# Optimization experiments

Measured on AMD Instinct MI355X. Metric: run time of the kernel, lower is better.

The kernel has to match this reference:

```python
import jax, jax.numpy as jnp
import numpy as np

EPS = 1e-8

def rms_norm(x, g):
    xf = x.astype(jnp.float32)
    ms = jnp.mean(xf * xf, axis=-1, keepdims=True)
    return (g * (xf * jax.lax.rsqrt(ms + EPS))).astype(x.dtype)

def setup_inputs() -> dict:
    key = jax.random.key(0)
    ks = jax.random.split(key, 10)
    B, S, D, H = 2, 2048, 1024, 16
    x = jax.random.normal(ks[0], (B, S, D), dtype=jnp.float32)
    p_bias = jax.random.normal(ks[1], (H, S, S), dtype=jnp.float32) * 0.02
    # additive causal mask [S, S]
    causal = jnp.tril(jnp.ones((S, S), dtype=bool))
    mask = jnp.where(causal, 0.0, -1e9).astype(jnp.float32)
    sd = 1.0 / np.sqrt(D)
    w_qkv = jax.random.normal(ks[2], (3 * D, D), dtype=jnp.float32) * sd
    w_u = jax.random.normal(ks[3], (D, D), dtype=jnp.float32) * sd
    g_ams = jnp.ones((D,), dtype=jnp.float32)
    w0 = jax.random.normal(ks[4], (D, D), dtype=jnp.float32) * sd
    w1 = jax.random.normal(ks[5], (2 * D, D), dtype=jnp.float32) * sd
    w3 = jax.random.normal(ks[6], (D, D), dtype=jnp.float32) * sd
    g_mffn = jnp.ones((D,), dtype=jnp.float32)
    return {"x": x, "p_bias": p_bias, "mask": mask, "w_qkv": w_qkv,
            "w_u": w_u, "g_ams": g_ams, "w0": w0, "w1": w1, "w3": w3,
            "g_mffn": g_mffn}

def reference(x, p_bias, mask, w_qkv, w_u, g_ams, w0, w1, w3, g_mffn):
    B, S, D = x.shape
    H = p_bias.shape[0]
    Dh = D // H
    scale = Dh ** -0.5
    # ---- AMS layer ----
    xn = rms_norm(x, g_ams)
    qkv = (xn @ w_qkv.T).reshape(B, S, 3, H, Dh)
    q, k, v = qkv[:, :, 0], qkv[:, :, 1], qkv[:, :, 2]  # [B,S,H,Dh]
    # scores: [B,H,S,S]
    score = jnp.einsum('bqhd,bkhd->bhqk', q, k) * scale
    score = score + p_bias[None] + mask[None, None]
    prob = jax.nn.silu(score)
    attn = jnp.einsum('bhqk,bkhd->bqhd', prob, v).reshape(B, S, D)
    u = jax.nn.silu(xn @ w_u.T)
    ams_out = attn * u
    # ---- MFFN layer ----
    o = ams_out @ w0.T + x
    on = rms_norm(o, g_mffn)
    x12 = on @ w1.T
    x1, x2 = jnp.split(x12, 2, axis=-1)
    hidden = jax.nn.silu(x1) * x2
    return hidden @ w3.T + o
```

## Files before the change

### kernel.cpp

```cpp
#include <hip/hip_runtime.h>
#include <hip/hip_bf16.h>
#include <cstdint>
#include <cstddef>

typedef __bf16 bf16x8 __attribute__((ext_vector_type(8)));
typedef float  f32x4  __attribute__((ext_vector_type(4)));
using u16 = unsigned short;
using u32 = unsigned int;

__device__ __forceinline__ float b2f(u16 u) {
  u32 v = ((u32)u) << 16;
  float f; __builtin_memcpy(&f, &v, 4); return f;
}
__device__ __forceinline__ u16 f2b(float f) {
  u32 v; __builtin_memcpy(&v, &f, 4);
  u32 r = v + 0x7fffu + ((v >> 16) & 1u);
  return (u16)(r >> 16);
}
__device__ __forceinline__ float silu(float x) {
  return x / (1.f + __expf(-x));
}
__device__ __forceinline__ f32x4 zero4() { f32x4 v = {0.f,0.f,0.f,0.f}; return v; }

typedef __attribute__((address_space(1))) const void* gas_ptr;
typedef __attribute__((address_space(3))) void*       las_ptr;
__device__ __forceinline__ void async_copy16(const void* g, void* l) {
  __builtin_amdgcn_global_load_lds((gas_ptr)g, (las_ptr)l, 16, 0, 0);
}

__global__ __launch_bounds__(256) void cvt_kernel(
    const float* __restrict__ wqkv, const float* __restrict__ wu,
    const float* __restrict__ w0,   const float* __restrict__ w1,
    const float* __restrict__ w3,
    u16* bqkv, u16* bu, u16* b0, u16* b1, u16* b3)
{
  const int blk = blockIdx.x;
  const float* src; u16* dst; int base;
  if      (blk < 3072) { src = wqkv; dst = bqkv; base = blk; }
  else if (blk < 4096) { src = wu;   dst = bu;   base = blk - 3072; }
  else if (blk < 5120) { src = w0;   dst = b0;   base = blk - 4096; }
  else if (blk < 7168) { src = w1;   dst = b1;   base = blk - 5120; }
  else                 { src = w3;   dst = b3;   base = blk - 7168; }
  const size_t i = (size_t)base * 1024 + threadIdx.x * 4;
  float4 v = *(const float4*)(src + i);
  uint2 o;
  o.x = (u32)f2b(v.x) | ((u32)f2b(v.y) << 16);
  o.y = (u32)f2b(v.z) | ((u32)f2b(v.w) << 16);
  *(uint2*)(dst + i) = o;
}

template<int EPI>
__global__ __launch_bounds__(256) void gemm_bt(
    const u16* __restrict__ A, const u16* __restrict__ Bw,
    const float* __restrict__ res, void* __restrict__ Cp,
    int M, int N, int K)
{
  __shared__ u16 sA[128 * 32];
  __shared__ u16 sB[128 * 32];

  const int t    = threadIdx.x;
  const int wave = t >> 6, lane = t & 63;
  const int quad = lane >> 4, l16 = lane & 15;
  const int wm = wave >> 1, wn = wave & 1;

  const int nwg = gridDim.x * gridDim.y;
  const int bid = blockIdx.y * gridDim.x + blockIdx.x;
  const int v   = (bid & 7) * (nwg >> 3) + (bid >> 3);
  const int bx  = v % gridDim.x, by = v / gridDim.x;
  const int m0 = by * 128, n0 = bx * 128;

  const int arow = t >> 2, achunk = t & 3;
  const u16* gA = A  + (size_t)(m0 + arow) * K + achunk * 8;
  const u16* gB = Bw + (size_t)(n0 + arow) * K + achunk * 8;
  u16* lA = sA + t * 8;
  u16* lB = sB + t * 8;

  f32x4 acc[4][4];
#pragma unroll
  for (int i = 0; i < 4; i++)
#pragma unroll
    for (int j = 0; j < 4; j++) acc[i][j] = zero4();

  for (int kb = 0; kb < K; kb += 32) {
    async_copy16(gA + kb,                 lA);
    async_copy16(gA + kb + (size_t)64*K,  lA + 2048);
    async_copy16(gB + kb,                 lB);
    async_copy16(gB + kb + (size_t)64*K,  lB + 2048);
    __syncthreads();

    bf16x8 af[4], bfr[4];
#pragma unroll
    for (int mi = 0; mi < 4; mi++)
      af[mi]  = *(const bf16x8*)(sA + (wm*64 + mi*16 + l16)*32 + quad*8);
#pragma unroll
    for (int ni = 0; ni < 4; ni++)
      bfr[ni] = *(const bf16x8*)(sB + (wn*64 + ni*16 + l16)*32 + quad*8);
#pragma unroll
    for (int mi = 0; mi < 4; mi++)
#pragma unroll
      for (int ni = 0; ni < 4; ni++)
        acc[mi][ni] = __builtin_amdgcn_mfma_f32_16x16x32_bf16(af[mi], bfr[ni], acc[mi][ni], 0, 0, 0);
    __syncthreads();
  }

#pragma unroll
  for (int mi = 0; mi < 4; mi++) {
#pragma unroll
    for (int ni = 0; ni < 4; ni++) {
#pragma unroll
      for (int r = 0; r < 4; r++) {
        const int row = m0 + wm*64 + mi*16 + quad*4 + r;
        const int col = n0 + wn*64 + ni*16 + l16;
        const size_t idx = (size_t)row * N + col;
        float vv = acc[mi][ni][r];
        if constexpr (EPI == 0) {
          ((u16*)Cp)[idx] = f2b(vv);
        } else if constexpr (EPI == 1) {
          ((u16*)Cp)[idx] = f2b(silu(vv));
        } else {
          ((float*)Cp)[idx] = vv + res[idx];
        }
      }
    }
  }
}

template<int EPI>
__global__ __launch_bounds__(256) void gemm64_bt(
    const u16* __restrict__ A, const u16* __restrict__ Bw,
    const float* __restrict__ res, void* __restrict__ Cp,
    int M, int N, int K)
{
  __shared__ u16 sA[128 * 32];
  __shared__ u16 sB[ 64 * 32];

  const int t    = threadIdx.x;
  const int wave = t >> 6, lane = t & 63;
  const int quad = lane >> 4, l16 = lane & 15;
  const int wm = wave >> 1, wn = wave & 1;

  const int nwg = gridDim.x * gridDim.y;
  const int bid = blockIdx.y * gridDim.x + blockIdx.x;
  const int v   = (bid & 7) * (nwg >> 3) + (bid >> 3);
  const int bx  = v & (gridDim.x - 1), by = v / gridDim.x;
  const int m0 = by * 128, n0 = bx * 64;

  const int arow = t >> 2, achunk = t & 3;
  const u16* gA = A  + (size_t)(m0 + arow) * K + achunk * 8;
  const u16* gB = Bw + (size_t)(n0 + arow) * K + achunk * 8;
  u16* lA = sA + t * 8;
  u16* lB = sB + t * 8;

  f32x4 acc[4][2];
#pragma unroll
  for (int i = 0; i < 4; i++) { acc[i][0] = zero4(); acc[i][1] = zero4(); }

  for (int kb = 0; kb < K; kb += 32) {
    async_copy16(gA + kb,                 lA);
    async_copy16(gA + kb + (size_t)64*K,  lA + 2048);
    async_copy16(gB + kb,                 lB);
    __syncthreads();

    bf16x8 af[4], bfr[2];
#pragma unroll
    for (int mi = 0; mi < 4; mi++)
      af[mi]  = *(const bf16x8*)(sA + (wm*64 + mi*16 + l16)*32 + quad*8);
#pragma unroll
    for (int ni = 0; ni < 2; ni++)
      bfr[ni] = *(const bf16x8*)(sB + (wn*32 + ni*16 + l16)*32 + quad*8);
#pragma unroll
    for (int mi = 0; mi < 4; mi++)
#pragma unroll
      for (int ni = 0; ni < 2; ni++)
        acc[mi][ni] = __builtin_amdgcn_mfma_f32_16x16x32_bf16(af[mi], bfr[ni], acc[mi][ni], 0, 0, 0);
    __syncthreads();
  }

#pragma unroll
  for (int mi = 0; mi < 4; mi++) {
#pragma unroll
    for (int ni = 0; ni < 2; ni++) {
#pragma unroll
      for (int r = 0; r < 4; r++) {
        const int row = m0 + wm*64 + mi*16 + quad*4 + r;
        const int col = n0 + wn*32 + ni*16 + l16;
        const size_t idx = (size_t)row * N + col;
        float vv = acc[mi][ni][r];
        if constexpr (EPI == 1) {
          ((u16*)Cp)[idx] = f2b(silu(vv));
        } else {
          ((float*)Cp)[idx] = vv + res[idx];
        }
      }
    }
  }
}

__global__ __launch_bounds__(256) void gemm_glu(
    const u16* __restrict__ A, const u16* __restrict__ Bw,
    u16* __restrict__ hid, int K)
{
  __shared__ u16 sA [128 * 32];
  __shared__ u16 sB1[ 64 * 32];
  __shared__ u16 sB2[ 64 * 32];

  const int t    = threadIdx.x;
  const int wave = t >> 6, lane = t & 63;
  const int quad = lane >> 4, l16 = lane & 15;
  const int wm = wave >> 1, wn = wave & 1;

  const int nwg = gridDim.x * gridDim.y;
  const int bid = blockIdx.y * gridDim.x + blockIdx.x;
  const int v   = (bid & 7) * (nwg >> 3) + (bid >> 3);
  const int bx  = v & (gridDim.x - 1), by = v / gridDim.x;
  const int m0 = by * 128, n0 = bx * 64;

  const int arow = t >> 2, achunk = t & 3;
  const u16* gA  = A  + (size_t)(m0 + arow) * K + achunk * 8;
  const u16* gB1 = Bw + (size_t)(n0 + arow) * K + achunk * 8;
  const u16* gB2 = Bw + (size_t)(n0 + 1024 + arow) * K + achunk * 8;
  u16* lA  = sA  + t * 8;
  u16* lB1 = sB1 + t * 8;
  u16* lB2 = sB2 + t * 8;

  f32x4 acc1[4][2], acc2[4][2];
#pragma unroll
  for (int i = 0; i < 4; i++) {
    acc1[i][0] = zero4(); acc1[i][1] = zero4();
    acc2[i][0] = zero4(); acc2[i][1] = zero4();
  }

  for (int kb = 0; kb < K; kb += 32) {
    async_copy16(gA + kb,                 lA);
    async_copy16(gA + kb + (size_t)64*K,  lA + 2048);
    async_copy16(gB1 + kb,                lB1);
    async_copy16(gB2 + kb,                lB2);
    __syncthreads();

    bf16x8 af[4], b1f[2], b2f[2];
#pragma unroll
    for (int mi = 0; mi < 4; mi++)
      af[mi] = *(const bf16x8*)(sA + (wm*64 + mi*16 + l16)*32 + quad*8);
#pragma unroll
    for (int ni = 0; ni < 2; ni++) {
      b1f[ni] = *(const bf16x8*)(sB1 + (wn*32 + ni*16 + l16)*32 + quad*8);
      b2f[ni] = *(const bf16x8*)(sB2 + (wn*32 + ni*16 + l16)*32 + quad*8);
    }
#pragma unroll
    for (int mi = 0; mi < 4; mi++)
#pragma unroll
      for (int ni = 0; ni < 2; ni++) {
        acc1[mi][ni] = __builtin_amdgcn_mfma_f32_16x16x32_bf16(af[mi], b1f[ni], acc1[mi][ni], 0, 0, 0);
        acc2[mi][ni] = __builtin_amdgcn_mfma_f32_16x16x32_bf16(af[mi], b2f[ni], acc2[mi][ni], 0, 0, 0);
      }
    __syncthreads();
  }

#pragma unroll
  for (int mi = 0; mi < 4; mi++) {
#pragma unroll
    for (int ni = 0; ni < 2; ni++) {
#pragma unroll
      for (int r = 0; r < 4; r++) {
        const int row = m0 + wm*64 + mi*16 + quad*4 + r;
        const int col = n0 + wn*32 + ni*16 + l16;
        hid[(size_t)row * 1024 + col] = f2b(silu(acc1[mi][ni][r]) * acc2[mi][ni][r]);
      }
    }
  }
}

__global__ __launch_bounds__(256) void vtrans_kernel(
    const u16* __restrict__ qkv, u16* __restrict__ vt)
{
  __shared__ u16 tile[64][72];
  const int st = blockIdx.x, bh = blockIdx.y;
  const int b = bh >> 4, h = bh & 15;
  const int t = threadIdx.x;
#pragma unroll
  for (int i = 0; i < 2; i++) {
    const int c = i * 256 + t;
    const int row = c >> 3, cc = c & 7;
    uint4 v = *(const uint4*)(qkv + (size_t)(b*2048 + st*64 + row)*3072 + 2048 + h*64 + cc*8);
    *(uint4*)(&tile[row][cc*8]) = v;
  }
  __syncthreads();
#pragma unroll
  for (int i = 0; i < 2; i++) {
    const int c = i * 256 + t;
    const int dh = c >> 3, cc = c & 7;
    u16 tmp[8];
#pragma unroll
    for (int j = 0; j < 8; j++) tmp[j] = tile[cc*8 + j][dh];
    *(uint4*)(vt + ((size_t)bh*64 + dh)*2048 + st*64 + cc*8) = *(uint4*)tmp;
  }
}

__global__ __launch_bounds__(1024) void attn_kernel(
    const u16* __restrict__ qkv,
    const u16* __restrict__ vt,
    const float* __restrict__ p_bias,
    const u16* __restrict__ ub,
    u16* __restrict__ am_out)
{
  constexpr int S = 2048, D3 = 3072;
  __shared__ u16 sQ [128 * 64];
  __shared__ u16 sK [128 * 64];
  __shared__ u16 sVt[ 64 * 128];
  __shared__ u16 sP [128 * 128];

  const int t    = threadIdx.x;
  const int wave = t >> 6, lane = t & 63;
  const int quad = lane >> 4, l16 = lane & 15;
  const int p  = blockIdx.x & 7, bh = blockIdx.x >> 3;
  const int b  = bh >> 4, h = bh & 15;
  const int wsq = wave & 3, wsk = wave >> 2;
  const int wpq = wave & 3, wpd = wave >> 2;
  const float scale = 0.125f;

  const int srow8 = lane >> 3, sc8 = lane & 7;
  const int srow16 = lane >> 4, sc16 = lane & 15;

#pragma unroll 1
  for (int sel = 0; sel < 2; sel++) {
    const int qt = sel ? 15 - p : p;
    const int q0 = qt * 128;

    __syncthreads();
    {
      const int row = wave * 8 + srow8;
      const int gc  = sc8 ^ (row & 7);
      async_copy16(qkv + (size_t)(b*S + q0 + row)*D3 + h*64 + gc*8,
                   sQ + wave*512 + lane*8);
    }

    f32x4 oacc[2];
    oacc[0] = zero4(); oacc[1] = zero4();

    for (int kt = 0; kt <= qt; kt++) {
      const int k0 = kt * 128;
      __syncthreads();
      {
        const int row = wave * 8 + srow8;
        const int gc  = sc8 ^ (row & 7);
        async_copy16(qkv + (size_t)(b*S + k0 + row)*D3 + 1024 + h*64 + gc*8,
                     sK + wave*512 + lane*8);
        const int vrow = wave * 4 + srow16;
        const int vgc  = sc16 ^ (vrow & 15);
        async_copy16(vt + ((size_t)bh*64 + vrow)*2048 + k0 + vgc*8,
                     sVt + wave*512 + lane*8);
      }
      __syncthreads();

      float bias[2][2][4];
#pragma unroll
      for (int mi = 0; mi < 2; mi++)
#pragma unroll
        for (int ni = 0; ni < 2; ni++)
#pragma unroll
          for (int r = 0; r < 4; r++) {
            const int q = wsq*32 + mi*16 + quad*4 + r;
            const int k = wsk*32 + ni*16 + l16;
            bias[mi][ni][r] = p_bias[((size_t)h*S + q0 + q)*S + k0 + k];
          }

      bf16x8 aq[2][2], bk[2][2];
#pragma unroll
      for (int mi = 0; mi < 2; mi++)
#pragma unroll
        for (int kk = 0; kk < 2; kk++) {
          const int row = wsq*32 + mi*16 + l16;
          const int phys = (quad + kk*4) ^ (row & 7);
          aq[mi][kk] = *(const bf16x8*)(sQ + row*64 + phys*8);
        }
#pragma unroll
      for (int ni = 0; ni < 2; ni++)
#pragma unroll
        for (int kk = 0; kk < 2; kk++) {
          const int row = wsk*32 + ni*16 + l16;
          const int phys = (quad + kk*4) ^ (row & 7);
          bk[ni][kk] = *(const bf16x8*)(sK + row*64 + phys*8);
        }

      f32x4 sacc[2][2];
#pragma unroll
      for (int mi = 0; mi < 2; mi++)
#pragma unroll
        for (int ni = 0; ni < 2; ni++) {
          f32x4 s = zero4();
          s = __builtin_amdgcn_mfma_f32_16x16x32_bf16(aq[mi][0], bk[ni][0], s, 0, 0, 0);
          s = __builtin_amdgcn_mfma_f32_16x16x32_bf16(aq[mi][1], bk[ni][1], s, 0, 0, 0);
          sacc[mi][ni] = s;
        }

#pragma unroll
      for (int mi = 0; mi < 2; mi++)
#pragma unroll
        for (int ni = 0; ni < 2; ni++)
#pragma unroll
          for (int r = 0; r < 4; r++) {
            const int q = wsq*32 + mi*16 + quad*4 + r;
            const int k = wsk*32 + ni*16 + l16;
            const int qi = q0 + q, ki = k0 + k;
            float vv = sacc[mi][ni][r] * scale + bias[mi][ni][r];
            vv = (ki <= qi) ? silu(vv) : 0.f;
            const int pc = (k >> 3) ^ (q & 15);
            sP[q*128 + pc*8 + (k & 7)] = f2b(vv);
          }
      __syncthreads();

#pragma unroll
      for (int kk = 0; kk < 4; kk++) {
        bf16x8 ap[2], bv;
#pragma unroll
        for (int mi = 0; mi < 2; mi++) {
          const int row = wpq*32 + mi*16 + l16;
          const int phys = (quad + kk*4) ^ (row & 15);
          ap[mi] = *(const bf16x8*)(sP + row*128 + phys*8);
        }
        {
          const int row = wpd*16 + l16;
          const int phys = (quad + kk*4) ^ (row & 15);
          bv = *(const bf16x8*)(sVt + row*128 + phys*8);
        }
#pragma unroll
        for (int mi = 0; mi < 2; mi++)
          oacc[mi] = __builtin_amdgcn_mfma_f32_16x16x32_bf16(ap[mi], bv, oacc[mi], 0, 0, 0);
      }
    }

#pragma unroll
    for (int mi = 0; mi < 2; mi++)
#pragma unroll
      for (int r = 0; r < 4; r++) {
        const int q  = wpq*32 + mi*16 + quad*4 + r;
        const int dh = wpd*16 + l16;
        const size_t oidx = (size_t)(b*S + q0 + q)*1024 + h*64 + dh;
        am_out[oidx] = f2b(oacc[mi][r] * b2f(ub[oidx]));
      }
  }
}

__global__ __launch_bounds__(256) void rmsnorm_kernel(
    const float* __restrict__ x, const float* __restrict__ g, u16* __restrict__ out)
{
  const int row = blockIdx.x, t = threadIdx.x;
  const int wave = t >> 6, lane = t & 63;
  const size_t base = (size_t)row * 1024;
  float v[4];
#pragma unroll
  for (int i = 0; i < 4; i++) v[i] = x[base + i * 256 + t];
  float ss = v[0]*v[0] + v[1]*v[1] + v[2]*v[2] + v[3]*v[3];
#pragma unroll
  for (int off = 32; off; off >>= 1) ss += __shfl_down(ss, off);
  __shared__ float red[4];
  if (lane == 0) red[wave] = ss;
  __syncthreads();
  const float r = rsqrtf((red[0] + red[1] + red[2] + red[3]) * (1.f / 1024.f) + 1e-8f);
#pragma unroll
  for (int i = 0; i < 4; i++) {
    const int j = i * 256 + t;
    out[base + j] = f2b(g[j] * v[i] * r);
  }
}

extern "C" void kernel_launch(void* const* d_in, const int* in_sizes, int n_in,
                              void* d_out, int out_size, void* d_ws, size_t ws_size,
                              hipStream_t stream)
{
  const float* x      = (const float*)d_in[0];
  const float* pbias  = (const float*)d_in[1];
  const float* w_qkv  = (const float*)d_in[3];
  const float* w_u    = (const float*)d_in[4];
  const float* g_ams  = (const float*)d_in[5];
  const float* w0     = (const float*)d_in[6];
  const float* w1     = (const float*)d_in[7];
  const float* w3     = (const float*)d_in[8];
  const float* g_mffn = (const float*)d_in[9];

  constexpr int M = 4096, D = 1024;
  char* ws = (char*)d_ws;
  u16*   xn    = (u16*)ws;
  u16*   qkv   = (u16*)(ws + (8u  << 20));
  u16*   ubuf  = (u16*)(ws + (32u << 20));
  u16*   am    = (u16*)(ws + (40u << 20));
  float* obuf  = (float*)(ws + (48u << 20));
  u16*   vt    = (u16*)(ws + (48u << 20));
  u16*   bqkv  = (u16*)(ws + (64u << 20));
  u16*   bu    = (u16*)(ws + (70u << 20));
  u16*   b0    = (u16*)(ws + (72u << 20));
  u16*   b1    = (u16*)(ws + (74u << 20));
  u16*   b3    = (u16*)(ws + (78u << 20));

  cvt_kernel<<<8192, 256, 0, stream>>>(w_qkv, w_u, w0, w1, w3, bqkv, bu, b0, b1, b3);
  rmsnorm_kernel<<<M, 256, 0, stream>>>(x, g_ams, xn);
  gemm_bt<0><<<dim3(24, 32), 256, 0, stream>>>(xn, bqkv, nullptr, qkv, M, 3072, D);
  gemm64_bt<1><<<dim3(16, 32), 256, 0, stream>>>(xn, bu, nullptr, ubuf, M, D, D);
  vtrans_kernel<<<dim3(32, 32), 256, 0, stream>>>(qkv, vt);
  attn_kernel<<<256, 1024, 0, stream>>>(qkv, vt, pbias, ubuf, am);
  gemm64_bt<2><<<dim3(16, 32), 256, 0, stream>>>(am, b0, x, obuf, M, D, D);
  rmsnorm_kernel<<<M, 256, 0, stream>>>(obuf, g_mffn, ubuf);
  gemm_glu<<<dim3(16, 32), 256, 0, stream>>>(ubuf, b1, am, D);
  gemm64_bt<3><<<dim3(16, 32), 256, 0, stream>>>(am, b3, obuf, (float*)d_out, M, D, D);
}
```

Before: 601.9 us.

## Double-buffer K/V tiles and prefetch bias in attention loop

Adds double-buffered shared-memory tiles for K and V^T. The next tile's async copies are issued at the top of each iteration while the current tile is computed, and the next tile's p_bias values are prefetched into a second register set. The two __syncthreads per iteration become explicit waitcnt plus s_barrier, which hides global load latency behind the MFMA and SiLU work. The cost is more LDS per block, and the bias array is indexed by a runtime buffer index, which may push it to scratch memory.

```diff
diff --git a/kernel.cpp b/kernel.cpp
--- a/kernel.cpp
+++ b/kernel.cpp
@@ -305,8 +305,8 @@
 {
   constexpr int S = 2048, D3 = 3072;
   __shared__ u16 sQ [128 * 64];
-  __shared__ u16 sK [128 * 64];
-  __shared__ u16 sVt[ 64 * 128];
+  __shared__ u16 sK [2][128 * 64];
+  __shared__ u16 sVt[2][ 64 * 128];
   __shared__ u16 sP [128 * 128];
 
   const int t    = threadIdx.x;
@@ -321,50 +321,71 @@
   const int srow8 = lane >> 3, sc8 = lane & 7;
   const int srow16 = lane >> 4, sc16 = lane & 15;
 
+  const int krow = wave * 8 + srow8;
+  const int kgc  = sc8 ^ (krow & 7);
+  const int vrow = wave * 4 + srow16;
+  const int vgc  = sc16 ^ (vrow & 15);
+  const u16* gK0 = qkv + (size_t)(b*S + krow)*D3 + 1024 + h*64 + kgc*8;
+  const u16* gV0 = vt  + ((size_t)bh*64 + vrow)*2048 + vgc*8;
+  u16* lK0 = &sK[0][wave*512 + lane*8];
+  u16* lK1 = &sK[1][wave*512 + lane*8];
+  u16* lV0 = &sVt[0][wave*512 + lane*8];
+  u16* lV1 = &sVt[1][wave*512 + lane*8];
+
 #pragma unroll 1
   for (int sel = 0; sel < 2; sel++) {
     const int qt = sel ? 15 - p : p;
     const int q0 = qt * 128;
 
     __syncthreads();
+    async_copy16(qkv + (size_t)(b*S + q0 + krow)*D3 + h*64 + kgc*8,
+                 sQ + wave*512 + lane*8);
+    async_copy16(gK0, lK0);
+    async_copy16(gV0, lV0);
+
+    float breg[2][2][2][4];
     {
-      const int row = wave * 8 + srow8;
-      const int gc  = sc8 ^ (row & 7);
-      async_copy16(qkv + (size_t)(b*S + q0 + row)*D3 + h*64 + gc*8,
-                   sQ + wave*512 + lane*8);
+      const int bq = wsq*32 + quad*4;
+      const int bk = wsk*32 + l16;
+#pragma unroll
+      for (int mi = 0; mi < 2; mi++)
+#pragma unroll
+        for (int ni = 0; ni < 2; ni++)
+#pragma unroll
+          for (int r = 0; r < 4; r++)
+            breg[0][mi][ni][r] =
+              p_bias[((size_t)h*S + q0 + bq + mi*16 + r)*S + bk + ni*16];
     }
 
     f32x4 oacc[2];
     oacc[0] = zero4(); oacc[1] = zero4();
 
     for (int kt = 0; kt <= qt; kt++) {
+      const int cur = kt & 1;
+      const int cb  = kt & 1;
+
+      asm volatile("s_waitcnt vmcnt(0)" ::: "memory");
+      __builtin_amdgcn_s_barrier();
+
+      if (kt < qt) {
+        const size_t koff = (size_t)(kt + 1) * 128 * D3;
+        async_copy16(gK0 + koff, cur ? lK0 : lK1);
+        async_copy16(gV0 + (kt + 1) * 128, cur ? lV0 : lV1);
+        const int bq = wsq*32 + quad*4;
+        const int bk = wsk*32 + l16;
+#pragma unroll
+        for (int mi = 0; mi < 2; mi++)
+#pragma unroll
+          for (int ni = 0; ni < 2; ni++)
+#pragma unroll
+            for (int r = 0; r < 4; r++)
+              breg[cb ^ 1][mi][ni][r] =
+                p_bias[((size_t)h*S + q0 + bq + mi*16 + r)*S + (kt+1)*128 + bk + ni*16];
+      }
+
       const int k0 = kt * 128;
-      __syncthreads();
-      {
-        const int row = wave * 8 + srow8;
-        const int gc  = sc8 ^ (row & 7);
-        async_copy16(qkv + (size_t)(b*S + k0 + row)*D3 + 1024 + h*64 + gc*8,
-                     sK + wave*512 + lane*8);
-        const int vrow = wave * 4 + srow16;
-        const int vgc  = sc16 ^ (vrow & 15);
-        async_copy16(vt + ((size_t)bh*64 + vrow)*2048 + k0 + vgc*8,
-                     sVt + wave*512 + lane*8);
-      }
-      __syncthreads();
-
-      float bias[2][2][4];
-#pragma unroll
-      for (int mi = 0; mi < 2; mi++)
-#pragma unroll
-        for (int ni = 0; ni < 2; ni++)
-#pragma unroll
-          for (int r = 0; r < 4; r++) {
-            const int q = wsq*32 + mi*16 + quad*4 + r;
-            const int k = wsk*32 + ni*16 + l16;
-            bias[mi][ni][r] = p_bias[((size_t)h*S + q0 + q)*S + k0 + k];
-          }
-
-      bf16x8 aq[2][2], bk[2][2];
+
+      bf16x8 aq[2][2], bk2[2][2];
 #pragma unroll
       for (int mi = 0; mi < 2; mi++)
 #pragma unroll
@@ -379,7 +400,7 @@
         for (int kk = 0; kk < 2; kk++) {
           const int row = wsk*32 + ni*16 + l16;
           const int phys = (quad + kk*4) ^ (row & 7);
-          bk[ni][kk] = *(const bf16x8*)(sK + row*64 + phys*8);
+          bk2[ni][kk] = *(const bf16x8*)(&sK[cur][row*64 + phys*8]);
         }
 
       f32x4 sacc[2][2];
@@ -388,8 +409,8 @@
 #pragma unroll
         for (int ni = 0; ni < 2; ni++) {
           f32x4 s = zero4();
-          s = __builtin_amdgcn_mfma_f32_16x16x32_bf16(aq[mi][0], bk[ni][0], s, 0, 0, 0);
-          s = __builtin_amdgcn_mfma_f32_16x16x32_bf16(aq[mi][1], bk[ni][1], s, 0, 0, 0);
+          s = __builtin_amdgcn_mfma_f32_16x16x32_bf16(aq[mi][0], bk2[ni][0], s, 0, 0, 0);
+          s = __builtin_amdgcn_mfma_f32_16x16x32_bf16(aq[mi][1], bk2[ni][1], s, 0, 0, 0);
           sacc[mi][ni] = s;
         }
 
@@ -402,12 +423,13 @@
             const int q = wsq*32 + mi*16 + quad*4 + r;
             const int k = wsk*32 + ni*16 + l16;
             const int qi = q0 + q, ki = k0 + k;
-            float vv = sacc[mi][ni][r] * scale + bias[mi][ni][r];
+            float vv = sacc[mi][ni][r] * scale + breg[cb][mi][ni][r];
             vv = (ki <= qi) ? silu(vv) : 0.f;
             const int pc = (k >> 3) ^ (q & 15);
             sP[q*128 + pc*8 + (k & 7)] = f2b(vv);
           }
-      __syncthreads();
+      asm volatile("s_waitcnt lgkmcnt(0)" ::: "memory");
+      __builtin_amdgcn_s_barrier();
 
 #pragma unroll
       for (int kk = 0; kk < 4; kk++) {
@@ -421,7 +443,7 @@
         {
           const int row = wpd*16 + l16;
           const int phys = (quad + kk*4) ^ (row & 15);
-          bv = *(const bf16x8*)(sVt + row*128 + phys*8);
+          bv = *(const bf16x8*)(&sVt[cur][row*128 + phys*8]);
         }
 #pragma unroll
         for (int mi = 0; mi < 2; mi++)
```

Result: slower. 630.8 us (+4.8%).
